# Kernel tuning notes

Measured on AMD Instinct MI355X. Metric: run time of the kernel, lower is better.

The kernel has to match this reference:

```python
import jax, jax.numpy as jnp
import numpy as np

EPS = 1e-5
H = 16  # num_heads

def layer_norm(x, g, b):
    mu = jnp.mean(x, axis=-1, keepdims=True)
    var = jnp.mean(jnp.square(x - mu), axis=-1, keepdims=True)
    return (x - mu) * jax.lax.rsqrt(var + EPS) * g + b

def setup_inputs() -> dict:
    key = jax.random.key(0)
    ks = jax.random.split(key, 12)
    B, N, D, F = 4, 1024, 1024, 4096
    s = 0.02
    return {
        'x': jax.random.normal(ks[0], (B, N, D), jnp.float32),
        'ln1_g': jnp.ones((D,), jnp.float32), 'ln1_b': jnp.zeros((D,), jnp.float32),
        'Wq': s * jax.random.normal(ks[1], (D, D), jnp.float32), 'bq': jnp.zeros((D,), jnp.float32),
        'Wk': s * jax.random.normal(ks[2], (D, D), jnp.float32), 'bk': jnp.zeros((D,), jnp.float32),
        'Wv': s * jax.random.normal(ks[3], (D, D), jnp.float32), 'bv': jnp.zeros((D,), jnp.float32),
        'Wo': s * jax.random.normal(ks[4], (D, D), jnp.float32), 'bo': jnp.zeros((D,), jnp.float32),
        'ln2_g': jnp.ones((D,), jnp.float32), 'ln2_b': jnp.zeros((D,), jnp.float32),
        'W1': s * jax.random.normal(ks[5], (D, F), jnp.float32), 'b1': jnp.zeros((F,), jnp.float32),
        'W2': s * jax.random.normal(ks[6], (F, D), jnp.float32), 'b2': jnp.zeros((D,), jnp.float32),
        'pad_mask': jnp.zeros((B, N), jnp.bool_),
    }

def reference(x, ln1_g, ln1_b, Wq, bq, Wk, bk, Wv, bv, Wo, bo,
              ln2_g, ln2_b, W1, b1, W2, b2, pad_mask):
    B, N, D = x.shape
    c = D // H  # per-head channels
    h = layer_norm(x, ln1_g, ln1_b)
    q = (h @ Wq + bq).reshape(B, N, H, c).transpose(0, 2, 1, 3)  # b h n c
    k = (h @ Wk + bk).reshape(B, N, H, c).transpose(0, 2, 1, 3)
    v = (h @ Wv + bv).reshape(B, N, H, c).transpose(0, 2, 1, 3)
    q = q * (c ** -0.5)
    attn = jnp.einsum('bhic,bhjc->bhij', q, k)
    neg = -jnp.finfo(attn.dtype).max
    attn = jnp.where(pad_mask[:, None, None, :], neg, attn)
    causal = jnp.triu(jnp.ones((N, N), jnp.bool_), k=1)  # right-aligned, i==j
    attn = jnp.where(causal, neg, attn)
    attn = jax.nn.softmax(attn, axis=-1)
    o = jnp.einsum('bhij,bhjc->bhic', attn, v)
    o = o.transpose(0, 2, 1, 3).reshape(B, N, D)
    x = o @ Wo + bo + x  # attention residual
    m = layer_norm(x, ln2_g, ln2_b)
    m = jax.nn.gelu(m @ W1 + b1, approximate=False) @ W2 + b2
    return x + m
```

## Files before the change

### kernel.cpp

```cpp
#include <hip/hip_runtime.h>
#include <hip/hip_bf16.h>
#include <cmath>

typedef __bf16 bf16_t;
typedef __bf16 bf16x8 __attribute__((ext_vector_type(8)));
typedef __bf16 bf16x4 __attribute__((ext_vector_type(4)));
typedef float f32x4 __attribute__((ext_vector_type(4)));

#define AS1 __attribute__((address_space(1)))
#define AS3 __attribute__((address_space(3)))

__device__ __forceinline__ void async_lds16(const void* g, void* s) {
    __builtin_amdgcn_global_load_lds((const AS1 void*)g, (AS3 void*)s, 16, 0, 0);
}

__device__ __forceinline__ float bf2f(bf16_t v) { return (float)v; }

__device__ __forceinline__ void tile_coords(int gx, int gy, int& mb, int& nb) {
    const int nwg = gx * gy;
    int lin = blockIdx.y * gx + blockIdx.x;
    if ((nwg & 7) == 0) lin = (lin & 7) * (nwg >> 3) + (lin >> 3);
    if ((gx & 3) == 0 && (gy & 3) == 0) {
        const int st = lin >> 4, pos = lin & 15;
        const int stn = gx >> 2;
        mb = (st / stn) * 4 + (pos >> 2);
        nb = (st % stn) * 4 + (pos & 3);
    } else {
        mb = lin / gx; nb = lin % gx;
    }
}

__global__ __launch_bounds__(256) void k_prep(
    const float* __restrict__ s0, const float* __restrict__ s1,
    const float* __restrict__ s2, const float* __restrict__ s3,
    const float* __restrict__ s4, const float* __restrict__ s5,
    bf16_t* __restrict__ d0, bf16_t* __restrict__ d1, bf16_t* __restrict__ d2,
    bf16_t* __restrict__ d3, bf16_t* __restrict__ d4, bf16_t* __restrict__ d5,
    const float* __restrict__ x, const float* __restrict__ g,
    const float* __restrict__ bln, bf16_t* __restrict__ hout) {
    const int b = blockIdx.x;
    const int t = threadIdx.x;
    if (b >= 12288) {
        const int row = b - 12288;
        const float4 xv = reinterpret_cast<const float4*>(x + (size_t)row * 1024)[t];
        float s = xv.x + xv.y + xv.z + xv.w;
        float s2 = xv.x * xv.x + xv.y * xv.y + xv.z * xv.z + xv.w * xv.w;
#pragma unroll
        for (int mk = 32; mk >= 1; mk >>= 1) {
            s += __shfl_xor(s, mk);
            s2 += __shfl_xor(s2, mk);
        }
        __shared__ float red[8];
        const int w = t >> 6, l = t & 63;
        if (l == 0) { red[w] = s; red[4 + w] = s2; }
        __syncthreads();
        s = red[0] + red[1] + red[2] + red[3];
        s2 = red[4] + red[5] + red[6] + red[7];
        const float mu = s * (1.0f / 1024.0f);
        const float var = s2 * (1.0f / 1024.0f) - mu * mu;
        const float rs = rsqrtf(var + 1e-5f);
        const float4 gv = reinterpret_cast<const float4*>(g)[t];
        const float4 bv = reinterpret_cast<const float4*>(bln)[t];
        bf16x4 o4;
        o4[0] = (bf16_t)((xv.x - mu) * rs * gv.x + bv.x);
        o4[1] = (bf16_t)((xv.y - mu) * rs * gv.y + bv.y);
        o4[2] = (bf16_t)((xv.z - mu) * rs * gv.z + bv.z);
        o4[3] = (bf16_t)((xv.w - mu) * rs * gv.w + bv.w);
        *reinterpret_cast<bf16x4*>(hout + (size_t)row * 1024 + t * 4) = o4;
        return;
    }
    const float* src; bf16_t* dst; int R, C, gx, tile;
    if (b < 4096) {
        const int m = b >> 10; tile = b & 1023; gx = 32; R = 1024; C = 1024;
        src = m == 0 ? s0 : m == 1 ? s1 : m == 2 ? s2 : s3;
        dst = m == 0 ? d0 : m == 1 ? d1 : m == 2 ? d2 : d3;
    } else if (b < 8192) {
        tile = b - 4096; gx = 128; R = 1024; C = 4096; src = s4; dst = d4;
    } else {
        tile = b - 8192; gx = 32; R = 4096; C = 1024; src = s5; dst = d5;
    }
    const int r0 = (tile / gx) << 5, c0 = (tile % gx) << 5;
    __shared__ float tl[32][33];
    const int tx = t & 31, ty = t >> 5;
#pragma unroll
    for (int i = 0; i < 32; i += 8)
        tl[ty + i][tx] = src[(size_t)(r0 + ty + i) * C + c0 + tx];
    __syncthreads();
#pragma unroll
    for (int i = 0; i < 32; i += 8)
        dst[(size_t)(c0 + ty + i) * R + r0 + tx] = (bf16_t)tl[tx][ty + i];
}

__global__ __launch_bounds__(256) void k_reduce_ln4(
    const bf16_t* __restrict__ pp,
    const float* __restrict__ bo, const float* __restrict__ x,
    const float* __restrict__ g, const float* __restrict__ b,
    bf16_t* __restrict__ x2, bf16_t* __restrict__ m2, long long zs) {
    const int row = blockIdx.x;
    const int t = threadIdx.x;
    const size_t off = (size_t)row * 1024 + t * 4;
    const float4 bb = reinterpret_cast<const float4*>(bo)[t];
    const float4 xv = *reinterpret_cast<const float4*>(x + off);
    float4 v;
    v.x = bb.x + xv.x; v.y = bb.y + xv.y; v.z = bb.z + xv.z; v.w = bb.w + xv.w;
#pragma unroll
    for (int z = 0; z < 4; z++) {
        const bf16x4 p = *reinterpret_cast<const bf16x4*>(pp + z * zs + off);
        v.x += bf2f(p[0]); v.y += bf2f(p[1]); v.z += bf2f(p[2]); v.w += bf2f(p[3]);
    }
    bf16x4 xo;
    xo[0] = (bf16_t)v.x; xo[1] = (bf16_t)v.y; xo[2] = (bf16_t)v.z; xo[3] = (bf16_t)v.w;
    *reinterpret_cast<bf16x4*>(x2 + off) = xo;
    float s = v.x + v.y + v.z + v.w;
    float s2 = v.x * v.x + v.y * v.y + v.z * v.z + v.w * v.w;
#pragma unroll
    for (int mk = 32; mk >= 1; mk >>= 1) {
        s += __shfl_xor(s, mk);
        s2 += __shfl_xor(s2, mk);
    }
    __shared__ float red[8];
    const int w = t >> 6, l = t & 63;
    if (l == 0) { red[w] = s; red[4 + w] = s2; }
    __syncthreads();
    s = red[0] + red[1] + red[2] + red[3];
    s2 = red[4] + red[5] + red[6] + red[7];
    const float mu = s * (1.0f / 1024.0f);
    const float var = s2 * (1.0f / 1024.0f) - mu * mu;
    const float rs = rsqrtf(var + 1e-5f);
    const float4 gv = reinterpret_cast<const float4*>(g)[t];
    const float4 bv = reinterpret_cast<const float4*>(b)[t];
    bf16x4 o4;
    o4[0] = (bf16_t)((v.x - mu) * rs * gv.x + bv.x);
    o4[1] = (bf16_t)((v.y - mu) * rs * gv.y + bv.y);
    o4[2] = (bf16_t)((v.z - mu) * rs * gv.z + bv.z);
    o4[3] = (bf16_t)((v.w - mu) * rs * gv.w + bv.w);
    *reinterpret_cast<bf16x4*>(m2 + off) = o4;
}

__global__ __launch_bounds__(256) void k_reduce_out4(
    const bf16_t* __restrict__ pA, const bf16_t* __restrict__ pB,
    const float* __restrict__ b2, const bf16_t* __restrict__ x2,
    float* __restrict__ outp, long long zs) {
    const size_t off = ((size_t)blockIdx.x * 256 + threadIdx.x) * 4;
    const bf16x4 c = *reinterpret_cast<const bf16x4*>(x2 + off);
    const float4 bi = reinterpret_cast<const float4*>(b2)[(off >> 2) & 255];
    float4 v;
    v.x = bf2f(c[0]) + bi.x; v.y = bf2f(c[1]) + bi.y;
    v.z = bf2f(c[2]) + bi.z; v.w = bf2f(c[3]) + bi.w;
#pragma unroll
    for (int z = 0; z < 2; z++) {
        const bf16x4 a = *reinterpret_cast<const bf16x4*>(pA + z * zs + off);
        const bf16x4 b = *reinterpret_cast<const bf16x4*>(pB + z * zs + off);
        v.x += bf2f(a[0]) + bf2f(b[0]);
        v.y += bf2f(a[1]) + bf2f(b[1]);
        v.z += bf2f(a[2]) + bf2f(b[2]);
        v.w += bf2f(a[3]) + bf2f(b[3]);
    }
    *reinterpret_cast<float4*>(outp + off) = v;
}

enum { EPI_QKV = 0, EPI_GELU = 1, EPI_PARTB = 2 };

template <int EPI>
__global__ __launch_bounds__(256, 3) void k_gemm2(
    const bf16_t* __restrict__ A, const bf16_t* __restrict__ BT,
    const float* __restrict__ bias0, const float* __restrict__ bias1,
    const float* __restrict__ bias2,
    bf16_t* __restrict__ outB, bf16_t* __restrict__ outB2,
    bf16_t* __restrict__ outB3,
    int M, int N, int Ksub, int Kstr, long long zstride) {
    int mb, nb;
    tile_coords(gridDim.x, gridDim.y, mb, nb);
    const int mbase = mb * 128;
    const int nbase = nb * 128;

    const bf16_t* Ab = A + (size_t)blockIdx.z * Ksub;
    const bf16_t* Bb = BT + (size_t)blockIdx.z * Ksub;

    const int t = threadIdx.x;
    const int w = t >> 6, l = t & 63;
    const int wr = w >> 1, wc = w & 1;
    const int lrow = l & 15, lg = l >> 4;

    __shared__ alignas(16) bf16_t As[3][128 * 32];
    __shared__ alignas(16) bf16_t Bs[3][128 * 32];

    f32x4 acc[4][4] = {};

    const int sr = t >> 2;
    const int sc = t & 3;
    const int ssw = (sc ^ ((sr >> 1) & 3)) * 8;

    auto stage = [&](int ks, int buf) {
        const int k0 = ks << 5;
#pragma unroll
        for (int c = 0; c < 2; c++)
            async_lds16(Ab + (size_t)(mbase + c * 64 + sr) * Kstr + k0 + ssw,
                        &As[buf][c * 2048 + t * 8]);
#pragma unroll
        for (int c = 0; c < 2; c++)
            async_lds16(Bb + (size_t)(nbase + c * 64 + sr) * Kstr + k0 + ssw,
                        &Bs[buf][c * 2048 + t * 8]);
    };

    stage(0, 0);
    stage(1, 1);
    const int nt = Ksub >> 5;
    int cur = 0;
    for (int tt = 0; tt < nt; tt++) {
        asm volatile("s_waitcnt vmcnt(4)" ::: "memory");
        __builtin_amdgcn_sched_barrier(0);
        __builtin_amdgcn_s_barrier();
        __builtin_amdgcn_sched_barrier(0);
        if (tt + 2 < nt) {
            int nbuf = cur + 2; if (nbuf >= 3) nbuf -= 3;
            stage(tt + 2, nbuf);
        }
        bf16x8 a[4], b[4];
#pragma unroll
        for (int i = 0; i < 4; i++) {
            const int r = wr * 64 + i * 16 + lrow;
            a[i] = *reinterpret_cast<const bf16x8*>(
                &As[cur][r * 32 + ((lg ^ ((r >> 1) & 3)) * 8)]);
        }
#pragma unroll
        for (int j = 0; j < 4; j++) {
            const int r = wc * 64 + j * 16 + lrow;
            b[j] = *reinterpret_cast<const bf16x8*>(
                &Bs[cur][r * 32 + ((lg ^ ((r >> 1) & 3)) * 8)]);
        }
        __builtin_amdgcn_s_setprio(1);
#pragma unroll
        for (int i = 0; i < 4; i++)
#pragma unroll
            for (int j = 0; j < 4; j++)
                acc[i][j] = __builtin_amdgcn_mfma_f32_16x16x32_bf16(a[i], b[j], acc[i][j], 0, 0, 0);
        __builtin_amdgcn_s_setprio(0);
        cur = cur + 1; if (cur >= 3) cur = 0;
    }

#pragma unroll
    for (int i = 0; i < 4; i++) {
#pragma unroll
        for (int j = 0; j < 4; j++) {
            const int col = nbase + wc * 64 + j * 16 + lrow;
            float bj = 0.f;
            int kind = 0, cc = col;
            if constexpr (EPI == EPI_QKV) {
                kind = col >> 10; cc = col & 1023;
                bj = (kind == 0 ? bias0 : kind == 1 ? bias1 : bias2)[cc];
            } else if constexpr (EPI == EPI_GELU) {
                bj = bias0[col];
            }
#pragma unroll
            for (int r = 0; r < 4; r++) {
                const int row = mbase + wr * 64 + i * 16 + lg * 4 + r;
                const float v = acc[i][j][r] + bj;
                if constexpr (EPI == EPI_QKV) {
                    const int bidx = row >> 10, ns = row & 1023;
                    const int hh = cc >> 6, ch = cc & 63;
                    const int bhh = bidx * 16 + hh;
                    if (kind == 0)
                        outB[((size_t)bhh * 1024 + ns) * 64 + ch] = (bf16_t)(v * 0.125f);
                    else if (kind == 1)
                        outB2[((size_t)bhh * 1024 + ns) * 64 + ch] = (bf16_t)v;
                    else
                        outB3[((size_t)bhh * 64 + ch) * 1024 + ns] = (bf16_t)v;
                } else if constexpr (EPI == EPI_GELU) {
                    const float ge = 0.5f * v * (1.0f + erff(v * 0.70710678118654752f));
                    outB[(size_t)row * N + col] = (bf16_t)ge;
                } else {
                    bf16_t* po = (blockIdx.z < 2 ? outB : outB2) +
                                 (size_t)(blockIdx.z & 1) * zstride;
                    po[(size_t)row * N + col] = (bf16_t)v;
                }
            }
        }
    }
}

template <int EPI>
__global__ __launch_bounds__(512, 2) void k_gemm256(
    const bf16_t* __restrict__ A, const bf16_t* __restrict__ BT,
    const float* __restrict__ bias0,
    bf16_t* __restrict__ outB, bf16_t* __restrict__ outB2,
    int M, int N, int Ksub, int Kstr, long long zstride) {
    int mb, nb;
    tile_coords(gridDim.x, gridDim.y, mb, nb);
    const int mbase = mb * 256;
    const int nbase = nb * 256;

    const bf16_t* Ab = A + (size_t)blockIdx.z * Ksub;
    const bf16_t* Bb = BT + (size_t)blockIdx.z * Ksub;

    const int t = threadIdx.x;
    const int w = t >> 6, l = t & 63;
    const int wr = w >> 2, wc = w & 3;
    const int lrow = l & 15, lg = l >> 4;

    __shared__ alignas(16) bf16_t As[2][256 * 64];
    __shared__ alignas(16) bf16_t Bs[2][256 * 64];

    f32x4 acc[8][4] = {};

    const int sr = t >> 3;
    const int ssw = ((t & 7) ^ (sr & 7)) * 8;

    const bf16_t* pa = Ab + (size_t)(mbase + sr) * Kstr + ssw;
    const bf16_t* pb = Bb + (size_t)(nbase + sr) * Kstr + ssw;

    auto stageA = [&](int kt, int buf, int half) {
        const int k0 = kt << 6;
#pragma unroll
        for (int i = 0; i < 2; i++)
            async_lds16(pa + (size_t)((half * 2 + i) * 64) * Kstr + k0,
                        &As[buf][(half * 2 + i) * 4096 + t * 8]);
    };
    auto stageB = [&](int kt, int buf, int half) {
        const int k0 = kt << 6;
#pragma unroll
        for (int i = 0; i < 2; i++)
            async_lds16(pb + (size_t)((half * 2 + i) * 64) * Kstr + k0,
                        &Bs[buf][(half * 2 + i) * 4096 + t * 8]);
    };

    stageA(0, 0, 0); stageA(0, 0, 1); stageB(0, 0, 0); stageB(0, 0, 1);
    __syncthreads();
    const int nt = Ksub >> 6;
    for (int kt = 0; kt < nt; kt++) {
        const int cur = kt & 1;
        const bool pf = (kt + 1) < nt;
        if (pf) stageA(kt + 1, cur ^ 1, 0);
        bf16x8 bfr[4][2];
#pragma unroll
        for (int fj = 0; fj < 4; fj++) {
            const int rb = wc * 64 + fj * 16 + lrow;
#pragma unroll
            for (int ks = 0; ks < 2; ks++)
                bfr[fj][ks] = *reinterpret_cast<const bf16x8*>(
                    &Bs[cur][rb * 64 + (((ks * 4 + lg) ^ (rb & 7)) * 8)]);
        }
        if (pf) stageA(kt + 1, cur ^ 1, 1);
        {
            bf16x8 afr[4][2];
#pragma unroll
            for (int fi = 0; fi < 4; fi++) {
                const int ra = wr * 64 + fi * 16 + lrow;
#pragma unroll
                for (int ks = 0; ks < 2; ks++)
                    afr[fi][ks] = *reinterpret_cast<const bf16x8*>(
                        &As[cur][ra * 64 + (((ks * 4 + lg) ^ (ra & 7)) * 8)]);
            }
            __builtin_amdgcn_s_setprio(1);
#pragma unroll
            for (int fi = 0; fi < 4; fi++)
#pragma unroll
                for (int fj = 0; fj < 4; fj++)
#pragma unroll
                    for (int ks = 0; ks < 2; ks++)
                        acc[fi][fj] = __builtin_amdgcn_mfma_f32_16x16x32_bf16(
                            afr[fi][ks], bfr[fj][ks], acc[fi][fj], 0, 0, 0);
            __builtin_amdgcn_s_setprio(0);
        }
        if (pf) stageB(kt + 1, cur ^ 1, 0);
        {
            bf16x8 afr[4][2];
#pragma unroll
            for (int fi = 0; fi < 4; fi++) {
                const int ra = 128 + wr * 64 + fi * 16 + lrow;
#pragma unroll
                for (int ks = 0; ks < 2; ks++)
                    afr[fi][ks] = *reinterpret_cast<const bf16x8*>(
                        &As[cur][ra * 64 + (((ks * 4 + lg) ^ (ra & 7)) * 8)]);
            }
            if (pf) stageB(kt + 1, cur ^ 1, 1);
            __builtin_amdgcn_s_setprio(1);
#pragma unroll
            for (int fi = 0; fi < 4; fi++)
#pragma unroll
                for (int fj = 0; fj < 4; fj++)
#pragma unroll
                    for (int ks = 0; ks < 2; ks++)
                        acc[4 + fi][fj] = __builtin_amdgcn_mfma_f32_16x16x32_bf16(
                            afr[fi][ks], bfr[fj][ks], acc[4 + fi][fj], 0, 0, 0);
            __builtin_amdgcn_s_setprio(0);
        }
        __syncthreads();
    }

#pragma unroll
    for (int h = 0; h < 2; h++) {
#pragma unroll
        for (int fi = 0; fi < 4; fi++) {
#pragma unroll
            for (int fj = 0; fj < 4; fj++) {
                const int col = nbase + wc * 64 + fj * 16 + lrow;
                float bj = 0.f;
                if constexpr (EPI == EPI_GELU) bj = bias0[col];
#pragma unroll
                for (int r = 0; r < 4; r++) {
                    const int row = mbase + h * 128 + wr * 64 + fi * 16 + lg * 4 + r;
                    const float v = acc[h * 4 + fi][fj][r] + bj;
                    if constexpr (EPI == EPI_GELU) {
                        const float ge = 0.5f * v * (1.0f + erff(v * 0.70710678118654752f));
                        outB[(size_t)row * N + col] = (bf16_t)ge;
                    } else {
                        bf16_t* po = (blockIdx.z < 2 ? outB : outB2) +
                                     (size_t)(blockIdx.z & 1) * zstride;
                        po[(size_t)row * N + col] = (bf16_t)v;
                    }
                }
            }
        }
    }
}

__global__ __launch_bounds__(256, 4) void k_attn(
    const bf16_t* __restrict__ q, const bf16_t* __restrict__ kk,
    const bf16_t* __restrict__ vt, const unsigned char* __restrict__ pad,
    bf16_t* __restrict__ o) {
    const int qt = 15 - (blockIdx.x >> 6);
    const int bh = blockIdx.x & 63;
    const int bb = bh >> 4, hh = bh & 15;
    const int t = threadIdx.x;
    const int w = t >> 6, l = t & 63;
    const int lrow = l & 15, lg = l >> 4;
    const int qbase = qt * 64;

    __shared__ alignas(16) bf16_t Ks[2][64 * 64];
    __shared__ alignas(16) bf16_t Vs[2][64 * 64];
    __shared__ alignas(16) bf16_t Ps[4][16 * 64];
    __shared__ unsigned char padRow[1024];

    const size_t bh_off = (size_t)bh * 1024 * 64;
    *reinterpret_cast<uchar4*>(&padRow[t * 4]) =
        *reinterpret_cast<const uchar4*>(&pad[bb * 1024 + t * 4]);

    const int qrow = qbase + w * 16 + lrow;
    bf16x8 qf[2];
#pragma unroll
    for (int ks = 0; ks < 2; ks++)
        qf[ks] = *reinterpret_cast<const bf16x8*>(q + bh_off + (size_t)qrow * 64 + ks * 32 + lg * 8);

    f32x4 oacc[4] = {};
    float mrow[4] = {-1e30f, -1e30f, -1e30f, -1e30f};
    float lsum[4] = {0.f, 0.f, 0.f, 0.f};

    const int sr = t >> 3;
    const int ssw = ((t & 7) ^ (sr & 7)) * 8;

    auto stage = [&](int kb, int buf) {
        const bf16_t* kp = kk + bh_off + (size_t)kb * 64;
        async_lds16(kp + (size_t)sr * 64 + ssw, &Ks[buf][t * 8]);
        async_lds16(kp + (size_t)(32 + sr) * 64 + ssw, &Ks[buf][2048 + t * 8]);
        const bf16_t* vp = vt + bh_off + kb;
        async_lds16(vp + (size_t)sr * 1024 + ssw, &Vs[buf][t * 8]);
        async_lds16(vp + (size_t)(32 + sr) * 1024 + ssw, &Vs[buf][2048 + t * 8]);
    };

    stage(0, 0);
    asm volatile("s_waitcnt lgkmcnt(0)" ::: "memory");
    const int nkb = qt + 1;
    for (int ib = 0; ib < nkb; ib++) {
        const int cur = ib & 1;
        const int kb = ib * 64;
        asm volatile("s_waitcnt vmcnt(0)" ::: "memory");
        __builtin_amdgcn_sched_barrier(0);
        __builtin_amdgcn_s_barrier();
        __builtin_amdgcn_sched_barrier(0);
        if (ib + 1 < nkb) stage(kb + 64, cur ^ 1);

        f32x4 s[4] = {};
#pragma unroll
        for (int ks = 0; ks < 2; ks++) {
#pragma unroll
            for (int jt = 0; jt < 4; jt++) {
                const int kr = jt * 16 + lrow;
                bf16x8 bfr = *reinterpret_cast<const bf16x8*>(
                    &Ks[cur][kr * 64 + (((ks * 4 + lg) ^ (kr & 7)) * 8)]);
                s[jt] = __builtin_amdgcn_mfma_f32_16x16x32_bf16(qf[ks], bfr, s[jt], 0, 0, 0);
            }
        }
#pragma unroll
        for (int jt = 0; jt < 4; jt++) {
            const int kvg = kb + jt * 16 + lrow;
            const bool padm = padRow[kvg] != 0;
#pragma unroll
            for (int r = 0; r < 4; r++) {
                const int qg = qbase + w * 16 + lg * 4 + r;
                if (kvg > qg || padm) s[jt][r] = -1e30f;
            }
        }
        float mx[4];
#pragma unroll
        for (int r = 0; r < 4; r++) {
            float m0 = fmaxf(fmaxf(s[0][r], s[1][r]), fmaxf(s[2][r], s[3][r]));
#pragma unroll
            for (int mk = 8; mk >= 1; mk >>= 1) m0 = fmaxf(m0, __shfl_xor(m0, mk));
            mx[r] = m0;
        }
        const bool need = (mx[0] > mrow[0] + 8.f) || (mx[1] > mrow[1] + 8.f) ||
                          (mx[2] > mrow[2] + 8.f) || (mx[3] > mrow[3] + 8.f);
        if (__any(need)) {
#pragma unroll
            for (int r = 0; r < 4; r++) {
                const float mn = fmaxf(mrow[r], mx[r]);
                const float al = __expf(mrow[r] - mn);
                mrow[r] = mn;
                lsum[r] *= al;
#pragma unroll
                for (int ct = 0; ct < 4; ct++) oacc[ct][r] *= al;
            }
        }
#pragma unroll
        for (int jt = 0; jt < 4; jt++)
#pragma unroll
            for (int r = 0; r < 4; r++)
                s[jt][r] = __expf(s[jt][r] - mrow[r]);
#pragma unroll
        for (int r = 0; r < 4; r++) {
            float sm = s[0][r] + s[1][r] + s[2][r] + s[3][r];
#pragma unroll
            for (int mk = 8; mk >= 1; mk >>= 1) sm += __shfl_xor(sm, mk);
            lsum[r] += sm;
        }
#pragma unroll
        for (int jt = 0; jt < 4; jt++)
#pragma unroll
            for (int r = 0; r < 4; r++) {
                const int prow = lg * 4 + r;
                const int kvc = jt * 16 + lrow;
                Ps[w][prow * 64 + (((kvc >> 3) ^ (prow & 7)) * 8) + (kvc & 7)] = (bf16_t)s[jt][r];
            }
#pragma unroll
        for (int ks = 0; ks < 2; ks++) {
            bf16x8 pa = *reinterpret_cast<const bf16x8*>(
                &Ps[w][lrow * 64 + (((ks * 4 + lg) ^ (lrow & 7)) * 8)]);
#pragma unroll
            for (int ct = 0; ct < 4; ct++) {
                const int vr = ct * 16 + lrow;
                bf16x8 vb = *reinterpret_cast<const bf16x8*>(
                    &Vs[cur][vr * 64 + (((ks * 4 + lg) ^ (vr & 7)) * 8)]);
                oacc[ct] = __builtin_amdgcn_mfma_f32_16x16x32_bf16(pa, vb, oacc[ct], 0, 0, 0);
            }
        }
    }
#pragma unroll
    for (int ct = 0; ct < 4; ct++) {
#pragma unroll
        for (int r = 0; r < 4; r++) {
            const int qg = qbase + w * 16 + lg * 4 + r;
            const float val = oacc[ct][r] / lsum[r];
            o[((size_t)bb * 1024 + qg) * 1024 + hh * 64 + ct * 16 + lrow] = (bf16_t)val;
        }
    }
}

extern "C" void kernel_launch(void* const* d_in, const int* in_sizes, int n_in,
                              void* d_out, int out_size, void* d_ws, size_t ws_size,
                              hipStream_t stream) {
    const float* x    = (const float*)d_in[0];
    const float* ln1g = (const float*)d_in[1];
    const float* ln1b = (const float*)d_in[2];
    const float* Wq   = (const float*)d_in[3];
    const float* bq   = (const float*)d_in[4];
    const float* Wk   = (const float*)d_in[5];
    const float* bk   = (const float*)d_in[6];
    const float* Wv   = (const float*)d_in[7];
    const float* bv   = (const float*)d_in[8];
    const float* Wo   = (const float*)d_in[9];
    const float* bo   = (const float*)d_in[10];
    const float* ln2g = (const float*)d_in[11];
    const float* ln2b = (const float*)d_in[12];
    const float* W1   = (const float*)d_in[13];
    const float* b1   = (const float*)d_in[14];
    const float* W2   = (const float*)d_in[15];
    const float* b2   = (const float*)d_in[16];
    const unsigned char* pad = (const unsigned char*)d_in[17];

    char* ws = (char*)d_ws;
    const size_t MB = 1024 * 1024;
    bf16_t* WqkvT = (bf16_t*)(ws + 0 * MB);
    bf16_t* WoT = (bf16_t*)(ws + 6 * MB);
    bf16_t* W1T = (bf16_t*)(ws + 8 * MB);
    bf16_t* W2T = (bf16_t*)(ws + 16 * MB);
    bf16_t* h   = (bf16_t*)(ws + 24 * MB);
    bf16_t* qb  = (bf16_t*)(ws + 32 * MB);
    bf16_t* kb  = (bf16_t*)(ws + 40 * MB);
    bf16_t* vb  = (bf16_t*)(ws + 48 * MB);
    bf16_t* ob  = (bf16_t*)(ws + 56 * MB);
    bf16_t* ppO = (bf16_t*)(ws + 24 * MB);
    bf16_t* m2  = (bf16_t*)(ws + 56 * MB);
    bf16_t* x2  = (bf16_t*)(ws + 64 * MB);
    bf16_t* hid = (bf16_t*)(ws + 24 * MB);
    bf16_t* pW01 = (bf16_t*)(ws + 0 * MB);
    bf16_t* pW23 = (bf16_t*)(ws + 80 * MB);

    const long long ZS = 4ll * 1024 * 1024;

    const dim3 blk(256);
    const dim3 blk8(512);
    k_prep<<<16384, blk, 0, stream>>>(
        Wq, Wk, Wv, Wo, W1, W2,
        WqkvT, WqkvT + 1024 * 1024, WqkvT + 2048 * 1024, WoT, W1T, W2T,
        x, ln1g, ln1b, h);
    k_gemm2<EPI_QKV><<<dim3(24, 32), blk, 0, stream>>>(
        h, WqkvT, bq, bk, bv, qb, kb, vb, 4096, 3072, 1024, 1024, 0);
    k_attn<<<1024, blk, 0, stream>>>(qb, kb, vb, pad, ob);
    k_gemm2<EPI_PARTB><<<dim3(8, 32, 4), blk, 0, stream>>>(
        ob, WoT, nullptr, nullptr, nullptr, ppO, ppO + 2 * ZS, nullptr,
        4096, 1024, 256, 1024, ZS);
    k_reduce_ln4<<<4096, blk, 0, stream>>>(ppO, bo, x, ln2g, ln2b, x2, m2, ZS);
    k_gemm256<EPI_GELU><<<dim3(16, 16), blk8, 0, stream>>>(
        m2, W1T, b1, hid, nullptr, 4096, 4096, 1024, 1024, 0);
    k_gemm256<EPI_PARTB><<<dim3(4, 16, 4), blk8, 0, stream>>>(
        hid, W2T, nullptr, pW01, pW23, 4096, 1024, 1024, 4096, ZS);
    k_reduce_out4<<<4096, blk, 0, stream>>>(pW01, pW23, b2, x2, (float*)d_out, ZS);
}
```

Baseline: 225.7 us.

## Switch 256x256 GEMM to triple-buffered K=32 pipeline with one barrier per step

Measured after the change: 239.8 us. +6.3%, slower.

```diff
diff --git a/kernel.cpp b/kernel.cpp
--- a/kernel.cpp
+++ b/kernel.cpp
@@ -280,7 +280,7 @@
 }
 
 template <int EPI>
-__global__ __launch_bounds__(512, 2) void k_gemm256(
+__global__ __launch_bounds__(512, 1) void k_gemm256(
     const bf16_t* __restrict__ A, const bf16_t* __restrict__ BT,
     const float* __restrict__ bias0,
     bf16_t* __restrict__ outB, bf16_t* __restrict__ outB2,
@@ -298,94 +298,65 @@
     const int wr = w >> 2, wc = w & 3;
     const int lrow = l & 15, lg = l >> 4;
 
-    __shared__ alignas(16) bf16_t As[2][256 * 64];
-    __shared__ alignas(16) bf16_t Bs[2][256 * 64];
+    __shared__ alignas(16) bf16_t As[3][256 * 32];
+    __shared__ alignas(16) bf16_t Bs[3][256 * 32];
 
     f32x4 acc[8][4] = {};
 
-    const int sr = t >> 3;
-    const int ssw = ((t & 7) ^ (sr & 7)) * 8;
+    const int sr = t >> 2;
+    const int sc = t & 3;
+    const int ssw = (sc ^ ((sr >> 1) & 3)) * 8;
 
     const bf16_t* pa = Ab + (size_t)(mbase + sr) * Kstr + ssw;
     const bf16_t* pb = Bb + (size_t)(nbase + sr) * Kstr + ssw;
 
-    auto stageA = [&](int kt, int buf, int half) {
-        const int k0 = kt << 6;
-#pragma unroll
-        for (int i = 0; i < 2; i++)
-            async_lds16(pa + (size_t)((half * 2 + i) * 64) * Kstr + k0,
-                        &As[buf][(half * 2 + i) * 4096 + t * 8]);
+    auto stage = [&](int kt, int buf) {
+        const int k0 = kt << 5;
+        async_lds16(pa + k0, &As[buf][t * 8]);
+        async_lds16(pa + (size_t)128 * Kstr + k0, &As[buf][4096 + t * 8]);
+        async_lds16(pb + k0, &Bs[buf][t * 8]);
+        async_lds16(pb + (size_t)128 * Kstr + k0, &Bs[buf][4096 + t * 8]);
     };
-    auto stageB = [&](int kt, int buf, int half) {
-        const int k0 = kt << 6;
-#pragma unroll
-        for (int i = 0; i < 2; i++)
-            async_lds16(pb + (size_t)((half * 2 + i) * 64) * Kstr + k0,
-                        &Bs[buf][(half * 2 + i) * 4096 + t * 8]);
-    };
-
-    stageA(0, 0, 0); stageA(0, 0, 1); stageB(0, 0, 0); stageB(0, 0, 1);
-    __syncthreads();
-    const int nt = Ksub >> 6;
-    for (int kt = 0; kt < nt; kt++) {
-        const int cur = kt & 1;
-        const bool pf = (kt + 1) < nt;
-        if (pf) stageA(kt + 1, cur ^ 1, 0);
-        bf16x8 bfr[4][2];
+
+    stage(0, 0);
+    stage(1, 1);
+    const int nt = Ksub >> 5;
+    int cur = 0;
+    for (int tt = 0; tt < nt; tt++) {
+        asm volatile("s_waitcnt vmcnt(4)" ::: "memory");
+        __builtin_amdgcn_sched_barrier(0);
+        __builtin_amdgcn_s_barrier();
+        __builtin_amdgcn_sched_barrier(0);
+        if (tt + 2 < nt) {
+            int nbuf = cur + 2; if (nbuf >= 3) nbuf -= 3;
+            stage(tt + 2, nbuf);
+        }
+        bf16x8 bfr[4];
 #pragma unroll
         for (int fj = 0; fj < 4; fj++) {
             const int rb = wc * 64 + fj * 16 + lrow;
-#pragma unroll
-            for (int ks = 0; ks < 2; ks++)
-                bfr[fj][ks] = *reinterpret_cast<const bf16x8*>(
-                    &Bs[cur][rb * 64 + (((ks * 4 + lg) ^ (rb & 7)) * 8)]);
-        }
-        if (pf) stageA(kt + 1, cur ^ 1, 1);
-        {
-            bf16x8 afr[4][2];
+            bfr[fj] = *reinterpret_cast<const bf16x8*>(
+                &Bs[cur][rb * 32 + ((lg ^ ((rb >> 1) & 3)) * 8)]);
+        }
+#pragma unroll
+        for (int h = 0; h < 2; h++) {
+            bf16x8 afr[4];
 #pragma unroll
             for (int fi = 0; fi < 4; fi++) {
-                const int ra = wr * 64 + fi * 16 + lrow;
-#pragma unroll
-                for (int ks = 0; ks < 2; ks++)
-                    afr[fi][ks] = *reinterpret_cast<const bf16x8*>(
-                        &As[cur][ra * 64 + (((ks * 4 + lg) ^ (ra & 7)) * 8)]);
+                const int ra = h * 128 + wr * 64 + fi * 16 + lrow;
+                afr[fi] = *reinterpret_cast<const bf16x8*>(
+                    &As[cur][ra * 32 + ((lg ^ ((ra >> 1) & 3)) * 8)]);
             }
             __builtin_amdgcn_s_setprio(1);
 #pragma unroll
             for (int fi = 0; fi < 4; fi++)
 #pragma unroll
                 for (int fj = 0; fj < 4; fj++)
-#pragma unroll
-                    for (int ks = 0; ks < 2; ks++)
-                        acc[fi][fj] = __builtin_amdgcn_mfma_f32_16x16x32_bf16(
-                            afr[fi][ks], bfr[fj][ks], acc[fi][fj], 0, 0, 0);
+                    acc[h * 4 + fi][fj] = __builtin_amdgcn_mfma_f32_16x16x32_bf16(
+                        afr[fi], bfr[fj], acc[h * 4 + fi][fj], 0, 0, 0);
             __builtin_amdgcn_s_setprio(0);
         }
-        if (pf) stageB(kt + 1, cur ^ 1, 0);
-        {
-            bf16x8 afr[4][2];
-#pragma unroll
-            for (int fi = 0; fi < 4; fi++) {
-                const int ra = 128 + wr * 64 + fi * 16 + lrow;
-#pragma unroll
-                for (int ks = 0; ks < 2; ks++)
-                    afr[fi][ks] = *reinterpret_cast<const bf16x8*>(
-                        &As[cur][ra * 64 + (((ks * 4 + lg) ^ (ra & 7)) * 8)]);
-            }
-            if (pf) stageB(kt + 1, cur ^ 1, 1);
-            __builtin_amdgcn_s_setprio(1);
-#pragma unroll
-            for (int fi = 0; fi < 4; fi++)
-#pragma unroll
-                for (int fj = 0; fj < 4; fj++)
-#pragma unroll
-                    for (int ks = 0; ks < 2; ks++)
-                        acc[4 + fi][fj] = __builtin_amdgcn_mfma_f32_16x16x32_bf16(
-                            afr[fi][ks], bfr[fj][ks], acc[4 + fi][fj], 0, 0, 0);
-            __builtin_amdgcn_s_setprio(0);
-        }
-        __syncthreads();
+        cur = cur + 1; if (cur >= 3) cur = 0;
     }
 
 #pragma unroll
```

## Move W1/W2 transpose-convert into attention launch to fill idle CUs

Applied to the files above, without the earlier changes.

After: 222.3 us (median of 2 runs). About the same (-1.5%).

```diff
diff --git a/kernel.cpp b/kernel.cpp
--- a/kernel.cpp
+++ b/kernel.cpp
@@ -33,15 +33,14 @@
 __global__ __launch_bounds__(256) void k_prep(
     const float* __restrict__ s0, const float* __restrict__ s1,
     const float* __restrict__ s2, const float* __restrict__ s3,
-    const float* __restrict__ s4, const float* __restrict__ s5,
     bf16_t* __restrict__ d0, bf16_t* __restrict__ d1, bf16_t* __restrict__ d2,
-    bf16_t* __restrict__ d3, bf16_t* __restrict__ d4, bf16_t* __restrict__ d5,
+    bf16_t* __restrict__ d3,
     const float* __restrict__ x, const float* __restrict__ g,
     const float* __restrict__ bln, bf16_t* __restrict__ hout) {
     const int b = blockIdx.x;
     const int t = threadIdx.x;
-    if (b >= 12288) {
-        const int row = b - 12288;
+    if (b >= 4096) {
+        const int row = b - 4096;
         const float4 xv = reinterpret_cast<const float4*>(x + (size_t)row * 1024)[t];
         float s = xv.x + xv.y + xv.z + xv.w;
         float s2 = xv.x * xv.x + xv.y * xv.y + xv.z * xv.z + xv.w * xv.w;
@@ -69,26 +68,20 @@
         *reinterpret_cast<bf16x4*>(hout + (size_t)row * 1024 + t * 4) = o4;
         return;
     }
-    const float* src; bf16_t* dst; int R, C, gx, tile;
-    if (b < 4096) {
-        const int m = b >> 10; tile = b & 1023; gx = 32; R = 1024; C = 1024;
-        src = m == 0 ? s0 : m == 1 ? s1 : m == 2 ? s2 : s3;
-        dst = m == 0 ? d0 : m == 1 ? d1 : m == 2 ? d2 : d3;
-    } else if (b < 8192) {
-        tile = b - 4096; gx = 128; R = 1024; C = 4096; src = s4; dst = d4;
-    } else {
-        tile = b - 8192; gx = 32; R = 4096; C = 1024; src = s5; dst = d5;
-    }
-    const int r0 = (tile / gx) << 5, c0 = (tile % gx) << 5;
+    const int m = b >> 10;
+    const int tile = b & 1023;
+    const float* src = m == 0 ? s0 : m == 1 ? s1 : m == 2 ? s2 : s3;
+    bf16_t* dst = m == 0 ? d0 : m == 1 ? d1 : m == 2 ? d2 : d3;
+    const int r0 = (tile >> 5) << 5, c0 = (tile & 31) << 5;
     __shared__ float tl[32][33];
     const int tx = t & 31, ty = t >> 5;
 #pragma unroll
     for (int i = 0; i < 32; i += 8)
-        tl[ty + i][tx] = src[(size_t)(r0 + ty + i) * C + c0 + tx];
+        tl[ty + i][tx] = src[(size_t)(r0 + ty + i) * 1024 + c0 + tx];
     __syncthreads();
 #pragma unroll
     for (int i = 0; i < 32; i += 8)
-        dst[(size_t)(c0 + ty + i) * R + r0 + tx] = (bf16_t)tl[tx][ty + i];
+        dst[(size_t)(c0 + ty + i) * 1024 + r0 + tx] = (bf16_t)tl[tx][ty + i];
 }
 
 __global__ __launch_bounds__(256) void k_reduce_ln4(
@@ -418,19 +411,40 @@
 __global__ __launch_bounds__(256, 4) void k_attn(
     const bf16_t* __restrict__ q, const bf16_t* __restrict__ kk,
     const bf16_t* __restrict__ vt, const unsigned char* __restrict__ pad,
-    bf16_t* __restrict__ o) {
-    const int qt = 15 - (blockIdx.x >> 6);
-    const int bh = blockIdx.x & 63;
-    const int bb = bh >> 4, hh = bh & 15;
+    bf16_t* __restrict__ o,
+    const float* __restrict__ W1, const float* __restrict__ W2,
+    bf16_t* __restrict__ W1T, bf16_t* __restrict__ W2T) {
     const int t = threadIdx.x;
-    const int w = t >> 6, l = t & 63;
-    const int lrow = l & 15, lg = l >> 4;
-    const int qbase = qt * 64;
 
     __shared__ alignas(16) bf16_t Ks[2][64 * 64];
     __shared__ alignas(16) bf16_t Vs[2][64 * 64];
     __shared__ alignas(16) bf16_t Ps[4][16 * 64];
     __shared__ unsigned char padRow[1024];
+
+    if (blockIdx.x >= 1024) {
+        const int b = blockIdx.x - 1024;
+        const float* src; bf16_t* dst; int R, C, gxx, tile;
+        if (b < 4096) { tile = b; gxx = 128; R = 1024; C = 4096; src = W1; dst = W1T; }
+        else { tile = b - 4096; gxx = 32; R = 4096; C = 1024; src = W2; dst = W2T; }
+        const int r0 = (tile / gxx) << 5, c0 = (tile % gxx) << 5;
+        float* tl = reinterpret_cast<float*>(Ks);
+        const int tx = t & 31, ty = t >> 5;
+#pragma unroll
+        for (int i = 0; i < 32; i += 8)
+            tl[(ty + i) * 33 + tx] = src[(size_t)(r0 + ty + i) * C + c0 + tx];
+        __syncthreads();
+#pragma unroll
+        for (int i = 0; i < 32; i += 8)
+            dst[(size_t)(c0 + ty + i) * R + r0 + tx] = (bf16_t)tl[tx * 33 + ty + i];
+        return;
+    }
+
+    const int qt = 15 - (blockIdx.x >> 6);
+    const int bh = blockIdx.x & 63;
+    const int bb = bh >> 4, hh = bh & 15;
+    const int w = t >> 6, l = t & 63;
+    const int lrow = l & 15, lg = l >> 4;
+    const int qbase = qt * 64;
 
     const size_t bh_off = (size_t)bh * 1024 * 64;
     *reinterpret_cast<uchar4*>(&padRow[t * 4]) =
@@ -600,13 +614,13 @@
 
     const dim3 blk(256);
     const dim3 blk8(512);
-    k_prep<<<16384, blk, 0, stream>>>(
-        Wq, Wk, Wv, Wo, W1, W2,
-        WqkvT, WqkvT + 1024 * 1024, WqkvT + 2048 * 1024, WoT, W1T, W2T,
+    k_prep<<<8192, blk, 0, stream>>>(
+        Wq, Wk, Wv, Wo,
+        WqkvT, WqkvT + 1024 * 1024, WqkvT + 2048 * 1024, WoT,
         x, ln1g, ln1b, h);
     k_gemm2<EPI_QKV><<<dim3(24, 32), blk, 0, stream>>>(
         h, WqkvT, bq, bk, bv, qb, kb, vb, 4096, 3072, 1024, 1024, 0);
-    k_attn<<<1024, blk, 0, stream>>>(qb, kb, vb, pad, ob);
+    k_attn<<<9216, blk, 0, stream>>>(qb, kb, vb, pad, ob, W1, W2, W1T, W2T);
     k_gemm2<EPI_PARTB><<<dim3(8, 32, 4), blk, 0, stream>>>(
         ob, WoT, nullptr, nullptr, nullptr, ppO, ppO + 2 * ZS, nullptr,
         4096, 1024, 256, 1024, ZS);
```
